# Kernel optimization log

Hardware: AMD Instinct MI355X
Metric: run time of the kernel (lower is better)

Reference implementation:

```python
import jax, jax.numpy as jnp
import numpy as np

BATCH = 256
B_TYPES = 32   # input capsule types
C_TYPES = 10   # output capsule types
H, W = 8, 8    # input spatial extent == kernel (output is 1x1)
POSE = 16      # capsule pose length (shape (16,1))
NUM_ITER = 3
EPS = 1e-8


def setup_inputs() -> dict:
    key = jax.random.key(0)
    k1, k2, k3 = jax.random.split(key, 3)
    input_caps_poses = jax.random.normal(k1, (BATCH, B_TYPES, H, W, POSE, 1), jnp.float32)
    input_caps_activations = jax.random.uniform(k2, (BATCH, B_TYPES, H, W), jnp.float32)
    # nn.init.normal_(std=0.1) on [B, kh, kw, C, os0, is0]
    weight = 0.1 * jax.random.normal(k3, (B_TYPES, H, W, C_TYPES, POSE, POSE), jnp.float32)
    # routing_bias initialized to 0.1: [C, oh, ow, os0, os1]
    routing_bias = jnp.full((C_TYPES, 1, 1, POSE, 1), 0.1, jnp.float32)
    return {
        "input_caps_poses": input_caps_poses,
        "input_caps_activations": input_caps_activations,
        "weight": weight,
        "routing_bias": routing_bias,
    }


def _squash(s):
    # Hinton squash: ||s||^2/(1+||s||^2) * s/||s||, norm over pose dims
    n2 = jnp.sum(s * s, axis=(-2, -1), keepdims=True)
    return (n2 / (1.0 + n2)) * s * jax.lax.rsqrt(n2 + EPS)


def reference(input_caps_poses, input_caps_activations, weight, routing_bias):
    b = input_caps_poses.shape[0]
    # votes[b,c,B,h,w,o,p] = sum_i W[B,h,w,c,o,i] * pose[b,B,h,w,i,p]
    votes = jnp.einsum('Bhwcoi,bBhwip->bcBhwop', weight, input_caps_poses)
    logits = jnp.zeros((b, C_TYPES, B_TYPES, H, W), votes.dtype)
    bias = routing_bias.reshape(1, C_TYPES, POSE, 1)
    v = None
    for it in range(NUM_ITER):
        # coupling coefficients: softmax over output capsule types
        c = jax.nn.softmax(logits, axis=1)                      # [b,C,B,h,w]
        # weighted sum of votes over all input capsules (B,h,w)
        s = jnp.einsum('bcBhw,bcBhwop->bcop', c, votes) + bias  # [b,C,16,1]
        v = _squash(s)
        if it < NUM_ITER - 1:
            # agreement: dot(vote, output pose)
            logits = logits + jnp.einsum('bcBhwop,bcop->bcBhw', votes, v)
    output_caps_poses = v[:, :, None, None, :, :]               # [b,C,1,1,16,1]
    output_caps_activations = jnp.sqrt(
        jnp.sum(v * v, axis=(-2, -1)) + EPS)[:, :, None, None]  # [b,C,1,1]
    return output_caps_poses, output_caps_activations
```

## Files before the change

kernel.cpp:

```cpp
#include <hip/hip_runtime.h>
#include <hip/hip_fp16.h>
#include <math.h>


typedef _Float16 f16;
typedef _Float16 f16x8 __attribute__((ext_vector_type(8)));
typedef float f32x4 __attribute__((ext_vector_type(4)));

#define DPP_ADD(v, ctrl) ((v) + __int_as_float(__builtin_amdgcn_update_dpp( \
    0, __float_as_int(v), (ctrl), 0xF, 0xF, true)))

constexpr int LIT = 4;

template<int FIRST>
__global__ __launch_bounds__(256)
void pass_k(const float* __restrict__ poses, const float* __restrict__ weight,
            const float* __restrict__ vsum, float* __restrict__ s_out)
{
    __shared__ f16  Ws[640 * 24];
    __shared__ f16  xs[64 * 72];
    __shared__ float cfs[4][16 * 44];

    const int tid  = threadIdx.x;
    const int ngrp = blockIdx.x >> 2;
    const int bgrp = blockIdx.x & 3;
    const int b0   = bgrp * 64;

    const int wave = tid >> 6;
    const int lane = tid & 63;
    const int q    = lane >> 4;
    const int lo   = lane & 15;
    const int wtb  = wave * 16;
    const int bg   = b0 + wtb;
    float* cf = cfs[wave];

    float4 wreg[10];
    float4 xreg[4];
    const int b_loc = tid >> 2, part = tid & 3;

    auto load_iter = [&](int l) {
        const float* wp = weight + (size_t)(ngrp * LIT + l) * 10240;
        #pragma unroll
        for (int k = 0; k < 10; ++k)
            wreg[k] = ((const float4*)wp)[tid + k * 256];
        const float* xp = poses + (size_t)(b0 + b_loc) * 32768 + (size_t)(ngrp * LIT + l) * 64 + part * 16;
        #pragma unroll
        for (int j = 0; j < 4; ++j)
            xreg[j] = ((const float4*)xp)[j];
    };
    auto store_iter = [&]() {
        #pragma unroll
        for (int k = 0; k < 10; ++k) {
            const int f = tid + k * 256;
            f16* lp = Ws + (f >> 2) * 24 + (f & 3) * 4;
            lp[0] = (f16)wreg[k].x; lp[1] = (f16)wreg[k].y;
            lp[2] = (f16)wreg[k].z; lp[3] = (f16)wreg[k].w;
        }
        f16* lp = xs + b_loc * 72 + part * 16;
        #pragma unroll
        for (int j = 0; j < 4; ++j) {
            lp[4*j+0] = (f16)xreg[j].x; lp[4*j+1] = (f16)xreg[j].y;
            lp[4*j+2] = (f16)xreg[j].z; lp[4*j+3] = (f16)xreg[j].w;
        }
    };

    float vs[10][4];
    if (!FIRST) {
        #pragma unroll
        for (int c = 0; c < 10; ++c)
            #pragma unroll
            for (int r = 0; r < 4; ++r)
                vs[c][r] = vsum[((size_t)(bg + q*4 + r) * 10 + c) * 16 + lo];
    }

    const f32x4 zf = {0.f, 0.f, 0.f, 0.f};
    const f16x8 za = {0,0,0,0,0,0,0,0};
    const bool kglo = (q < 2);
    const int  i0a  = (q & 1) * 8;
    const int  nl0  = q >> 1;
    const int  i0b  = (q & 1) * 8;

    f32x4 acc[10];
    #pragma unroll
    for (int c = 0; c < 10; ++c) acc[c] = zf;

    load_iter(0);

    for (int l = 0; l < LIT; ++l) {
        __syncthreads();
        store_iter();
        if (l + 1 < LIT) load_iter(l + 1);
        __syncthreads();

        if (!FIRST) {
            f16x8 a_n[4];
            #pragma unroll
            for (int n = 0; n < 4; ++n) {
                f16x8 ax = *(const f16x8*)&xs[(wtb + lo) * 72 + n * 16 + i0a];
                a_n[n] = kglo ? ax : za;
            }
            #pragma unroll
            for (int n = 0; n < 4; ++n) {
                #pragma unroll
                for (int c = 0; c < 10; ++c) {
                    f16x8 bx = *(const f16x8*)&Ws[((n * 10 + c) * 16 + lo) * 24 + i0a];
                    f16x8 bf = kglo ? bx : za;
                    f32x4 V = __builtin_amdgcn_mfma_f32_16x16x32_f16(a_n[n], bf, zf, 0, 0, 0);
                    float p0 = V[0] * vs[c][0];
                    float p1 = V[1] * vs[c][1];
                    float p2 = V[2] * vs[c][2];
                    float p3 = V[3] * vs[c][3];
                    p0 = DPP_ADD(p0, 0x128); p0 = DPP_ADD(p0, 0x124); p0 = DPP_ADD(p0, 0x122); p0 = DPP_ADD(p0, 0x121);
                    p1 = DPP_ADD(p1, 0x128); p1 = DPP_ADD(p1, 0x124); p1 = DPP_ADD(p1, 0x122); p1 = DPP_ADD(p1, 0x121);
                    p2 = DPP_ADD(p2, 0x128); p2 = DPP_ADD(p2, 0x124); p2 = DPP_ADD(p2, 0x122); p2 = DPP_ADD(p2, 0x121);
                    p3 = DPP_ADD(p3, 0x128); p3 = DPP_ADD(p3, 0x124); p3 = DPP_ADD(p3, 0x122); p3 = DPP_ADD(p3, 0x121);
                    if (lo == 0) {
                        cf[(q*4 + 0) * 44 + n * 10 + c] = p0;
                        cf[(q*4 + 1) * 44 + n * 10 + c] = p1;
                        cf[(q*4 + 2) * 44 + n * 10 + c] = p2;
                        cf[(q*4 + 3) * 44 + n * 10 + c] = p3;
                    }
                }
            }
            {
                const int rb = lane >> 2;
                const int rn = lane & 3;
                float lg[10];
                #pragma unroll
                for (int c = 0; c < 10; ++c) lg[c] = cf[rb * 44 + rn * 10 + c];
                float m = lg[0];
                #pragma unroll
                for (int c = 1; c < 10; ++c) m = fmaxf(m, lg[c]);
                float sum = 0.f;
                #pragma unroll
                for (int c = 0; c < 10; ++c) { lg[c] = __expf(lg[c] - m); sum += lg[c]; }
                const float inv = 1.f / sum;
                #pragma unroll
                for (int c = 0; c < 10; ++c) cf[rb * 44 + rn * 10 + c] = lg[c] * inv;
            }
        }

        #pragma unroll
        for (int c = 0; c < 10; ++c) {
            #pragma unroll
            for (int np = 0; np < 2; ++np) {
                const int n_loc = np * 2 + nl0;
                f16x8 xa = *(const f16x8*)&xs[(wtb + lo) * 72 + n_loc * 16 + i0b];
                f16 ch;
                if (FIRST) ch = (f16)0.1f;
                else       ch = (f16)cf[lo * 44 + n_loc * 10 + c];
                f16x8 av = xa * ch;
                f16x8 bw = *(const f16x8*)&Ws[((n_loc * 10 + c) * 16 + lo) * 24 + i0b];
                acc[c] = __builtin_amdgcn_mfma_f32_16x16x32_f16(av, bw, acc[c], 0, 0, 0);
            }
        }
    }

    #pragma unroll
    for (int c = 0; c < 10; ++c) {
        float* sp = s_out + ((size_t)(bg + q * 4) * 10 + c) * 16 + lo;
        unsafeAtomicAdd(sp + 0 * 160, acc[c][0]);
        unsafeAtomicAdd(sp + 1 * 160, acc[c][1]);
        unsafeAtomicAdd(sp + 2 * 160, acc[c][2]);
        unsafeAtomicAdd(sp + 3 * 160, acc[c][3]);
    }
}

__global__ __launch_bounds__(256)
void squash_k(float* __restrict__ s, const float* __restrict__ bias,
              float* __restrict__ vsum, float* __restrict__ out, const int final_it)
{
    const int t = blockIdx.x * 256 + threadIdx.x;
    if (t >= 2560) return;
    const int c = t % 10;
    float* sp = s + (size_t)t * 16;
    const float* bp = bias + c * 16;
    float sv[16];
    float n2 = 0.f;
    #pragma unroll
    for (int o = 0; o < 16; ++o) { float v = sp[o] + bp[o]; sv[o] = v; n2 += v * v; }
    const float scale = n2 / (1.f + n2) * rsqrtf(n2 + 1e-8f);
    if (!final_it) {
        float* vp = vsum + (size_t)t * 16;
        #pragma unroll
        for (int o = 0; o < 16; ++o) { vp[o] += scale * sv[o]; sp[o] = 0.f; }
    } else {
        float a2 = 0.f;
        #pragma unroll
        for (int o = 0; o < 16; ++o) {
            float v = scale * sv[o];
            out[(size_t)t * 16 + o] = v;
            a2 += v * v;
        }
        out[40960 + t] = sqrtf(a2 + 1e-8f);
    }
}

extern "C" void kernel_launch(void* const* d_in, const int* in_sizes, int n_in,
                              void* d_out, int out_size, void* d_ws, size_t ws_size,
                              hipStream_t stream)
{
    const float* poses  = (const float*)d_in[0];
    const float* weight = (const float*)d_in[2];
    const float* bias   = (const float*)d_in[3];
    float* out  = (float*)d_out;
    float* s    = (float*)d_ws;
    float* vsum = s + 40960;

    hipMemsetAsync(d_ws, 0, 2 * 40960 * sizeof(float), stream);

    pass_k<1><<<512, 256, 0, stream>>>(poses, weight, vsum, s);
    squash_k<<<10, 256, 0, stream>>>(s, bias, vsum, out, 0);
    pass_k<0><<<512, 256, 0, stream>>>(poses, weight, vsum, s);
    squash_k<<<10, 256, 0, stream>>>(s, bias, vsum, out, 0);
    pass_k<0><<<512, 256, 0, stream>>>(poses, weight, vsum, s);
    squash_k<<<10, 256, 0, stream>>>(s, bias, vsum, out, 1);
}
```

Before: 220.9 us.

## Fuse squash into routing passes and compute agreement logits via 16x16x16 MFMA with fdot2

The intermediate squash kernels go away. Each pass now recomputes the squashed output poses from the previous raw s buffers, with bias added, in its prologue, using three separate s buffers. The agreement logits move off the K-padded 16x16x32 MFMA, DPP reductions and shared-memory softmax staging: they now use an unpadded 16x16x16 MFMA, fp16 dot2 against packed v, xor-shuffle reductions, and a register-resident softmax. This removes two kernel launches, the zero-padding waste and the LDS round trips. In exchange it adds redundant squash work per block and lowers the precision of the agreement dot product to fp16.

```diff
diff --git a/kernel.cpp b/kernel.cpp
--- a/kernel.cpp
+++ b/kernel.cpp
@@ -4,130 +4,146 @@
 
 
 typedef _Float16 f16;
+typedef _Float16 f16x2 __attribute__((ext_vector_type(2)));
+typedef _Float16 f16x4 __attribute__((ext_vector_type(4)));
 typedef _Float16 f16x8 __attribute__((ext_vector_type(8)));
+typedef __fp16   h16x2 __attribute__((ext_vector_type(2)));
 typedef float f32x4 __attribute__((ext_vector_type(4)));
 
 #define DPP_ADD(v, ctrl) ((v) + __int_as_float(__builtin_amdgcn_update_dpp( \
     0, __float_as_int(v), (ctrl), 0xF, 0xF, true)))
 
-constexpr int LIT = 4;
-
-template<int FIRST>
+__device__ __forceinline__ f16x2 pk(float a, float b) {
+    h16x2 t = __builtin_amdgcn_cvt_pkrtz(a, b);
+    return __builtin_bit_cast(f16x2, t);
+}
+
+#if __has_builtin(__builtin_amdgcn_fdot2)
+__device__ __forceinline__ float FDOT2(f16x2 a, f16x2 b, float c) {
+    return __builtin_amdgcn_fdot2(__builtin_bit_cast(h16x2, a),
+                                  __builtin_bit_cast(h16x2, b), c, false);
+}
+#else
+__device__ __forceinline__ float FDOT2(f16x2 a, f16x2 b, float c) {
+    return c + (float)a[0] * (float)b[0] + (float)a[1] * (float)b[1];
+}
+#endif
+
+constexpr int WS_ROW = 28;
+constexpr int XS_ROW = 76;
+
+__device__ __forceinline__ float xorsum4(float v) {
+    v += __shfl_xor(v, 16, 64);
+    v += __shfl_xor(v, 32, 64);
+    return v;
+}
+
+__device__ __forceinline__ f16x4 cvt4(float4 w) {
+    f16x2 a = pk(w.x, w.y);
+    f16x2 b = pk(w.z, w.w);
+    f16x4 r; r[0] = a[0]; r[1] = a[1]; r[2] = b[0]; r[3] = b[1];
+    return r;
+}
+
+template<int PASS>
 __global__ __launch_bounds__(256)
 void pass_k(const float* __restrict__ poses, const float* __restrict__ weight,
-            const float* __restrict__ vsum, float* __restrict__ s_out)
+            const float* __restrict__ bias,
+            const float* __restrict__ sp0, const float* __restrict__ sp1,
+            float* __restrict__ s_dst)
 {
-    __shared__ f16  Ws[640 * 24];
-    __shared__ f16  xs[64 * 72];
-    __shared__ float cfs[4][16 * 44];
+    __shared__ f16 Ws[640 * WS_ROW];
+    __shared__ f16 xs[64 * XS_ROW];
 
     const int tid  = threadIdx.x;
-    const int ngrp = blockIdx.x >> 2;
-    const int bgrp = blockIdx.x & 3;
-    const int b0   = bgrp * 64;
-
+    const int blk  = blockIdx.x;
+    const int ngrp = blk >> 2;
+    const int b0   = (blk & 3) * 64;
     const int wave = tid >> 6;
     const int lane = tid & 63;
     const int q    = lane >> 4;
     const int lo   = lane & 15;
     const int wtb  = wave * 16;
     const int bg   = b0 + wtb;
-    float* cf = cfs[wave];
+    const int nl0  = q >> 1;
+    const int iq   = (q & 1) * 8;
+
+    f16x2 vsp[10][2];
+    if (PASS >= 1) {
+        const int rowb = (bg + lo) * 10;
+        #pragma unroll
+        for (int c = 0; c < 10; ++c) {
+            float4 bb = *(const float4*)(bias + c * 16 + q * 4);
+            float4 sa = *(const float4*)(sp0 + (size_t)(rowb + c) * 16 + q * 4);
+            float t0 = sa.x + bb.x, t1 = sa.y + bb.y, t2 = sa.z + bb.z, t3 = sa.w + bb.w;
+            float n2 = xorsum4(t0*t0 + t1*t1 + t2*t2 + t3*t3);
+            float sc = n2 / (1.f + n2) * rsqrtf(n2 + 1e-8f);
+            float v0 = sc*t0, v1 = sc*t1, v2 = sc*t2, v3 = sc*t3;
+            if (PASS == 2) {
+                float4 sb = *(const float4*)(sp1 + (size_t)(rowb + c) * 16 + q * 4);
+                float u0 = sb.x + bb.x, u1 = sb.y + bb.y, u2 = sb.z + bb.z, u3 = sb.w + bb.w;
+                float m2 = xorsum4(u0*u0 + u1*u1 + u2*u2 + u3*u3);
+                float sc2 = m2 / (1.f + m2) * rsqrtf(m2 + 1e-8f);
+                v0 += sc2*u0; v1 += sc2*u1; v2 += sc2*u2; v3 += sc2*u3;
+            }
+            vsp[c][0] = pk(v0, v1);
+            vsp[c][1] = pk(v2, v3);
+        }
+    }
 
     float4 wreg[10];
     float4 xreg[4];
     const int b_loc = tid >> 2, part = tid & 3;
 
     auto load_iter = [&](int l) {
-        const float* wp = weight + (size_t)(ngrp * LIT + l) * 10240;
-        #pragma unroll
-        for (int k = 0; k < 10; ++k)
-            wreg[k] = ((const float4*)wp)[tid + k * 256];
-        const float* xp = poses + (size_t)(b0 + b_loc) * 32768 + (size_t)(ngrp * LIT + l) * 64 + part * 16;
-        #pragma unroll
-        for (int j = 0; j < 4; ++j)
-            xreg[j] = ((const float4*)xp)[j];
+        const float* wp = weight + (size_t)(ngrp * 4 + l) * 10240;
+        #pragma unroll
+        for (int k = 0; k < 10; ++k) wreg[k] = ((const float4*)wp)[tid + k * 256];
+        const float* xp = poses + (size_t)(b0 + b_loc) * 32768
+                          + (size_t)(ngrp * 16 + l * 4 + part) * 16;
+        #pragma unroll
+        for (int j = 0; j < 4; ++j) xreg[j] = ((const float4*)xp)[j];
     };
     auto store_iter = [&]() {
         #pragma unroll
         for (int k = 0; k < 10; ++k) {
             const int f = tid + k * 256;
-            f16* lp = Ws + (f >> 2) * 24 + (f & 3) * 4;
-            lp[0] = (f16)wreg[k].x; lp[1] = (f16)wreg[k].y;
-            lp[2] = (f16)wreg[k].z; lp[3] = (f16)wreg[k].w;
-        }
-        f16* lp = xs + b_loc * 72 + part * 16;
-        #pragma unroll
-        for (int j = 0; j < 4; ++j) {
-            lp[4*j+0] = (f16)xreg[j].x; lp[4*j+1] = (f16)xreg[j].y;
-            lp[4*j+2] = (f16)xreg[j].z; lp[4*j+3] = (f16)xreg[j].w;
-        }
+            *(f16x4*)&Ws[(f >> 2) * WS_ROW + (f & 3) * 4] = cvt4(wreg[k]);
+        }
+        f16* lp = xs + b_loc * XS_ROW + part * 16;
+        #pragma unroll
+        for (int j = 0; j < 4; ++j) *(f16x4*)&lp[j * 4] = cvt4(xreg[j]);
     };
 
-    float vs[10][4];
-    if (!FIRST) {
-        #pragma unroll
-        for (int c = 0; c < 10; ++c)
-            #pragma unroll
-            for (int r = 0; r < 4; ++r)
-                vs[c][r] = vsum[((size_t)(bg + q*4 + r) * 10 + c) * 16 + lo];
-    }
-
-    const f32x4 zf = {0.f, 0.f, 0.f, 0.f};
-    const f16x8 za = {0,0,0,0,0,0,0,0};
-    const bool kglo = (q < 2);
-    const int  i0a  = (q & 1) * 8;
-    const int  nl0  = q >> 1;
-    const int  i0b  = (q & 1) * 8;
-
     f32x4 acc[10];
     #pragma unroll
-    for (int c = 0; c < 10; ++c) acc[c] = zf;
+    for (int c = 0; c < 10; ++c) acc[c] = (f32x4){0.f, 0.f, 0.f, 0.f};
+
+    f16x2 cf[10][2];
 
     load_iter(0);
 
-    for (int l = 0; l < LIT; ++l) {
+    for (int l = 0; l < 4; ++l) {
         __syncthreads();
         store_iter();
-        if (l + 1 < LIT) load_iter(l + 1);
+        if (l + 1 < 4) load_iter(l + 1);
         __syncthreads();
 
-        if (!FIRST) {
-            f16x8 a_n[4];
+        if (PASS >= 1) {
+            float ce[10];
             #pragma unroll
             for (int n = 0; n < 4; ++n) {
-                f16x8 ax = *(const f16x8*)&xs[(wtb + lo) * 72 + n * 16 + i0a];
-                a_n[n] = kglo ? ax : za;
-            }
-            #pragma unroll
-            for (int n = 0; n < 4; ++n) {
+                f16x4 bx = *(const f16x4*)&xs[(wtb + lo) * XS_ROW + n * 16 + q * 4];
+                float lg[10];
                 #pragma unroll
                 for (int c = 0; c < 10; ++c) {
-                    f16x8 bx = *(const f16x8*)&Ws[((n * 10 + c) * 16 + lo) * 24 + i0a];
-                    f16x8 bf = kglo ? bx : za;
-                    f32x4 V = __builtin_amdgcn_mfma_f32_16x16x32_f16(a_n[n], bf, zf, 0, 0, 0);
-                    float p0 = V[0] * vs[c][0];
-                    float p1 = V[1] * vs[c][1];
-                    float p2 = V[2] * vs[c][2];
-                    float p3 = V[3] * vs[c][3];
-                    p0 = DPP_ADD(p0, 0x128); p0 = DPP_ADD(p0, 0x124); p0 = DPP_ADD(p0, 0x122); p0 = DPP_ADD(p0, 0x121);
-                    p1 = DPP_ADD(p1, 0x128); p1 = DPP_ADD(p1, 0x124); p1 = DPP_ADD(p1, 0x122); p1 = DPP_ADD(p1, 0x121);
-                    p2 = DPP_ADD(p2, 0x128); p2 = DPP_ADD(p2, 0x124); p2 = DPP_ADD(p2, 0x122); p2 = DPP_ADD(p2, 0x121);
-                    p3 = DPP_ADD(p3, 0x128); p3 = DPP_ADD(p3, 0x124); p3 = DPP_ADD(p3, 0x122); p3 = DPP_ADD(p3, 0x121);
-                    if (lo == 0) {
-                        cf[(q*4 + 0) * 44 + n * 10 + c] = p0;
-                        cf[(q*4 + 1) * 44 + n * 10 + c] = p1;
-                        cf[(q*4 + 2) * 44 + n * 10 + c] = p2;
-                        cf[(q*4 + 3) * 44 + n * 10 + c] = p3;
-                    }
+                    f16x4 aw = *(const f16x4*)&Ws[((n * 10 + c) * 16 + lo) * WS_ROW + q * 4];
+                    f32x4 D = __builtin_amdgcn_mfma_f32_16x16x16f16(
+                        aw, bx, (f32x4){0.f, 0.f, 0.f, 0.f}, 0, 0, 0);
+                    float p = FDOT2(pk(D[0], D[1]), vsp[c][0], 0.f);
+                    p = FDOT2(pk(D[2], D[3]), vsp[c][1], p);
+                    lg[c] = xorsum4(p);
                 }
-            }
-            {
-                const int rb = lane >> 2;
-                const int rn = lane & 3;
-                float lg[10];
-                #pragma unroll
-                for (int c = 0; c < 10; ++c) lg[c] = cf[rb * 44 + rn * 10 + c];
                 float m = lg[0];
                 #pragma unroll
                 for (int c = 1; c < 10; ++c) m = fmaxf(m, lg[c]);
@@ -135,22 +151,44 @@
                 #pragma unroll
                 for (int c = 0; c < 10; ++c) { lg[c] = __expf(lg[c] - m); sum += lg[c]; }
                 const float inv = 1.f / sum;
-                #pragma unroll
-                for (int c = 0; c < 10; ++c) cf[rb * 44 + rn * 10 + c] = lg[c] * inv;
+                if (n & 1) {
+                    #pragma unroll
+                    for (int c = 0; c < 10; ++c)
+                        cf[c][n >> 1] = pk(ce[c], lg[c] * inv);
+                } else {
+                    #pragma unroll
+                    for (int c = 0; c < 10; ++c) ce[c] = lg[c] * inv;
+                }
             }
         }
 
+        f16x8 xa[2];
+        #pragma unroll
+        for (int np = 0; np < 2; ++np) {
+            const f16* p = &xs[(wtb + lo) * XS_ROW + (np * 2 + nl0) * 16 + iq];
+            f16x4 x0 = *(const f16x4*)p;
+            f16x4 x1 = *(const f16x4*)(p + 4);
+            xa[np] = __builtin_shufflevector(x0, x1, 0, 1, 2, 3, 4, 5, 6, 7);
+        }
         #pragma unroll
         for (int c = 0; c < 10; ++c) {
             #pragma unroll
             for (int np = 0; np < 2; ++np) {
+                f16 ch;
+                if (PASS == 0) {
+                    ch = (f16)0.1f;
+                } else {
+                    union { f16x2 h; unsigned u; } cu; cu.h = cf[c][np];
+                    unsigned hv = nl0 ? (cu.u >> 16) : (cu.u & 0xffffu);
+                    union { unsigned short s; f16 h; } hu; hu.s = (unsigned short)hv;
+                    ch = hu.h;
+                }
                 const int n_loc = np * 2 + nl0;
-                f16x8 xa = *(const f16x8*)&xs[(wtb + lo) * 72 + n_loc * 16 + i0b];
-                f16 ch;
-                if (FIRST) ch = (f16)0.1f;
-                else       ch = (f16)cf[lo * 44 + n_loc * 10 + c];
-                f16x8 av = xa * ch;
-                f16x8 bw = *(const f16x8*)&Ws[((n_loc * 10 + c) * 16 + lo) * 24 + i0b];
+                const f16* wp_ = &Ws[((n_loc * 10 + c) * 16 + lo) * WS_ROW + iq];
+                f16x4 w0 = *(const f16x4*)wp_;
+                f16x4 w1 = *(const f16x4*)(wp_ + 4);
+                f16x8 bw = __builtin_shufflevector(w0, w1, 0, 1, 2, 3, 4, 5, 6, 7);
+                f16x8 av = xa[np] * ch;
                 acc[c] = __builtin_amdgcn_mfma_f32_16x16x32_f16(av, bw, acc[c], 0, 0, 0);
             }
         }
@@ -158,7 +196,7 @@
 
     #pragma unroll
     for (int c = 0; c < 10; ++c) {
-        float* sp = s_out + ((size_t)(bg + q * 4) * 10 + c) * 16 + lo;
+        float* sp = s_dst + ((size_t)(bg + q * 4) * 10 + c) * 16 + lo;
         unsafeAtomicAdd(sp + 0 * 160, acc[c][0]);
         unsafeAtomicAdd(sp + 1 * 160, acc[c][1]);
         unsafeAtomicAdd(sp + 2 * 160, acc[c][2]);
@@ -167,33 +205,27 @@
 }
 
 __global__ __launch_bounds__(256)
-void squash_k(float* __restrict__ s, const float* __restrict__ bias,
-              float* __restrict__ vsum, float* __restrict__ out, const int final_it)
+void epi_k(const float* __restrict__ s2, const float* __restrict__ bias,
+           float* __restrict__ out)
 {
     const int t = blockIdx.x * 256 + threadIdx.x;
     if (t >= 2560) return;
     const int c = t % 10;
-    float* sp = s + (size_t)t * 16;
+    const float* sp = s2 + (size_t)t * 16;
     const float* bp = bias + c * 16;
     float sv[16];
     float n2 = 0.f;
     #pragma unroll
     for (int o = 0; o < 16; ++o) { float v = sp[o] + bp[o]; sv[o] = v; n2 += v * v; }
     const float scale = n2 / (1.f + n2) * rsqrtf(n2 + 1e-8f);
-    if (!final_it) {
-        float* vp = vsum + (size_t)t * 16;
-        #pragma unroll
-        for (int o = 0; o < 16; ++o) { vp[o] += scale * sv[o]; sp[o] = 0.f; }
-    } else {
-        float a2 = 0.f;
-        #pragma unroll
-        for (int o = 0; o < 16; ++o) {
-            float v = scale * sv[o];
-            out[(size_t)t * 16 + o] = v;
-            a2 += v * v;
-        }
-        out[40960 + t] = sqrtf(a2 + 1e-8f);
-    }
+    float a2 = 0.f;
+    #pragma unroll
+    for (int o = 0; o < 16; ++o) {
+        float v = scale * sv[o];
+        out[(size_t)t * 16 + o] = v;
+        a2 += v * v;
+    }
+    out[40960 + t] = sqrtf(a2 + 1e-8f);
 }
 
 extern "C" void kernel_launch(void* const* d_in, const int* in_sizes, int n_in,
@@ -203,16 +235,15 @@
     const float* poses  = (const float*)d_in[0];
     const float* weight = (const float*)d_in[2];
     const float* bias   = (const float*)d_in[3];
-    float* out  = (float*)d_out;
-    float* s    = (float*)d_ws;
-    float* vsum = s + 40960;
-
-    hipMemsetAsync(d_ws, 0, 2 * 40960 * sizeof(float), stream);
-
-    pass_k<1><<<512, 256, 0, stream>>>(poses, weight, vsum, s);
-    squash_k<<<10, 256, 0, stream>>>(s, bias, vsum, out, 0);
-    pass_k<0><<<512, 256, 0, stream>>>(poses, weight, vsum, s);
-    squash_k<<<10, 256, 0, stream>>>(s, bias, vsum, out, 0);
-    pass_k<0><<<512, 256, 0, stream>>>(poses, weight, vsum, s);
-    squash_k<<<10, 256, 0, stream>>>(s, bias, vsum, out, 1);
-}
+    float* out = (float*)d_out;
+    float* s0 = (float*)d_ws;
+    float* s1 = s0 + 40960;
+    float* s2 = s1 + 40960;
+
+    (void)hipMemsetAsync(d_ws, 0, 3 * 40960 * sizeof(float), stream);
+
+    pass_k<0><<<512, 256, 0, stream>>>(poses, weight, bias, nullptr, nullptr, s0);
+    pass_k<1><<<512, 256, 0, stream>>>(poses, weight, bias, s0, nullptr, s1);
+    pass_k<2><<<512, 256, 0, stream>>>(poses, weight, bias, s0, s1, s2);
+    epi_k<<<10, 256, 0, stream>>>(s2, bias, out);
+}
```

Measured after the change: 204.7 us. -7.4%, faster.
